# Optimization experiments

Hardware: AMD Instinct MI355X
Metric: run time of the kernel (lower is better)

The kernel has to match this reference:

```python
import jax, jax.numpy as jnp
import numpy as np

EMBED_DIM = 1024
N_HEAD = 16
D_K = EMBED_DIM // N_HEAD


def setup_inputs() -> dict:
    key = jax.random.key(0)
    kq, kk, kv, kwq, kwk, kwv, kwo = jax.random.split(key, 7)
    B, S, E = 4, 2048, EMBED_DIM
    scale = 1.0 / np.sqrt(E)
    return {
        "Q": jax.random.normal(kq, (B, S, E), dtype=jnp.float32),
        "K": jax.random.normal(kk, (B, S, E), dtype=jnp.float32),
        "V": jax.random.normal(kv, (B, S, E), dtype=jnp.float32),
        "mask": jnp.zeros((1,), dtype=jnp.bool_),  # unused by the module's forward
        "Wq": jax.random.normal(kwq, (E, E), dtype=jnp.float32) * scale,
        "Wk": jax.random.normal(kwk, (E, E), dtype=jnp.float32) * scale,
        "Wv": jax.random.normal(kwv, (E, E), dtype=jnp.float32) * scale,
        "Wo": jax.random.normal(kwo, (E, E), dtype=jnp.float32) * scale,
    }


def reference(Q, K, V, mask, Wq, Wk, Wv, Wo):
    B, S, E = Q.shape
    H, Dk = N_HEAD, D_K
    # Linear projections (torch Linear: x @ W.T), split into heads -> [B,H,S,Dk]
    q = (Q @ Wq.T).reshape(B, S, H, Dk).transpose(0, 2, 1, 3)
    k = (K @ Wk.T).reshape(B, S, H, Dk).transpose(0, 2, 1, 3)
    v = (V @ Wv.T).reshape(B, S, H, Dk).transpose(0, 2, 1, 3)
    # Scaled dot-product attention (no mask is passed in the original forward;
    # dropout is identity in eval mode)
    scores = jnp.einsum("bhqd,bhkd->bhqk", q, k) / jnp.sqrt(jnp.float32(Dk))
    attn = jax.nn.softmax(scores, axis=-1)
    ctx = jnp.einsum("bhqk,bhkd->bhqd", attn, v)  # [B,H,S,Dk]
    ctx = ctx.transpose(0, 2, 1, 3).reshape(B, S, E)
    return ctx @ Wo.T
```

## Files before the change

kernel.cpp:

```cpp
#include <hip/hip_runtime.h>
#include <hip/hip_bf16.h>

#define B_  4
#define S_  2048
#define E_  1024
#define H_  16
#define DK_ 64
#define CSC 0.18033688011112042f

using bf16   = __bf16;
using bf16x8 = __attribute__((ext_vector_type(8))) __bf16;
using f32x4  = __attribute__((ext_vector_type(4))) float;

__device__ __forceinline__ f32x4 mfma16(bf16x8 a, bf16x8 b, f32x4 c) {
    return __builtin_amdgcn_mfma_f32_16x16x32_bf16(a, b, c, 0, 0, 0);
}

__device__ __forceinline__ bf16x8 cvt8(float4 a, float4 b) {
    bf16x8 r;
    r[0] = (bf16)a.x; r[1] = (bf16)a.y; r[2] = (bf16)a.z; r[3] = (bf16)a.w;
    r[4] = (bf16)b.x; r[5] = (bf16)b.y; r[6] = (bf16)b.z; r[7] = (bf16)b.w;
    return r;
}

__device__ __forceinline__ void gl16(const void* g, void* l) {
    __builtin_amdgcn_global_load_lds(
        (const __attribute__((address_space(1))) void*)g,
        (__attribute__((address_space(3))) void*)l, 16, 0, 0);
}

__global__ __launch_bounds__(256) void cvtw3(const float* __restrict__ a,
                                             const float* __restrict__ b,
                                             const float* __restrict__ c,
                                             bf16* __restrict__ d, float s0) {
    const int y = blockIdx.y;
    const float* s = y == 0 ? a : y == 1 ? b : c;
    const float sc = y == 0 ? s0 : 1.f;
    const size_t i = (size_t)blockIdx.x * 256 + threadIdx.x;
    float4 u = ((const float4*)s)[i * 2];
    float4 v = ((const float4*)s)[i * 2 + 1];
    u.x *= sc; u.y *= sc; u.z *= sc; u.w *= sc;
    v.x *= sc; v.y *= sc; v.z *= sc; v.w *= sc;
    ((bf16x8*)(d + (size_t)y * E_ * E_))[i] = cvt8(u, v);
}

__global__ __launch_bounds__(256, 3) void gemm_qkv(
    const float* __restrict__ Qi, const float* __restrict__ Ki,
    const float* __restrict__ Vi, const bf16* __restrict__ Wb,
    bf16* __restrict__ qws, bf16* __restrict__ kws, bf16* __restrict__ vtws) {
    __shared__ __align__(16) bf16 sA[128 * 32];
    __shared__ __align__(16) bf16 sB[128 * 32];

    const int t = threadIdx.x;
    const int lane = t & 63, wave = t >> 6;
    const int wm = wave >> 1, wn = wave & 1;
    const int quad = lane >> 4, l16 = lane & 15;

    const int sel = blockIdx.y >> 3;
    const int gm = blockIdx.x * 128;
    const int gn = (blockIdx.y & 7) * 128;

    const float* A = sel == 0 ? Qi : sel == 1 ? Ki : Vi;
    const bf16* W = Wb + (size_t)sel * E_ * E_;

    const int srow = t >> 1, scol = (t & 1) * 16;
    const float* ga = A + (size_t)(gm + srow) * E_ + scol;
    const int cb = (t & 1) * 2, swA = (srow >> 1) & 3;
    bf16* la0 = (bf16*)((char*)sA + srow * 64 + ((cb ^ swA) * 16));
    bf16* la1 = (bf16*)((char*)sA + srow * 64 + (((cb + 1) ^ swA) * 16));

    const int brow = lane >> 2;
    const int bcg  = (lane & 3) ^ ((lane >> 3) & 3);
    const bf16* gB[2];
#pragma unroll
    for (int j = 0; j < 2; ++j)
        gB[j] = W + (size_t)(gn + wave * 32 + j * 16 + brow) * E_ + bcg * 8;

    float4 ra[4];
#pragma unroll
    for (int j = 0; j < 4; ++j) ra[j] = *(const float4*)(ga + j * 4);

    f32x4 acc[4][4];
#pragma unroll
    for (int i = 0; i < 4; ++i)
#pragma unroll
        for (int j = 0; j < 4; ++j) acc[i][j] = f32x4{0.f, 0.f, 0.f, 0.f};

    for (int kt = 0; kt < E_ / 32; ++kt) {
        __syncthreads();
        *(bf16x8*)la0 = cvt8(ra[0], ra[1]);
        *(bf16x8*)la1 = cvt8(ra[2], ra[3]);
#pragma unroll
        for (int j = 0; j < 2; ++j)
            gl16(gB[j] + kt * 32, (char*)sB + (wave * 2 + j) * 1024);
        __syncthreads();
        if (kt + 1 < E_ / 32) {
            const int kk = (kt + 1) * 32;
#pragma unroll
            for (int j = 0; j < 4; ++j)
                ra[j] = *(const float4*)(ga + kk + j * 4);
        }

        bf16x8 Af[4], Bf[4];
#pragma unroll
        for (int ms = 0; ms < 4; ++ms) {
            const int r = wm * 64 + ms * 16 + l16;
            Af[ms] = *(const bf16x8*)((const char*)sA + r * 64 +
                                      ((quad ^ ((r >> 1) & 3)) * 16));
        }
#pragma unroll
        for (int ns = 0; ns < 4; ++ns) {
            const int r = wn * 64 + ns * 16 + l16;
            Bf[ns] = *(const bf16x8*)((const char*)sB + r * 64 +
                                      ((quad ^ ((r >> 1) & 3)) * 16));
        }
#pragma unroll
        for (int ms = 0; ms < 4; ++ms)
#pragma unroll
            for (int ns = 0; ns < 4; ++ns)
                acc[ms][ns] = mfma16(Af[ms], Bf[ns], acc[ms][ns]);
    }

#pragma unroll
    for (int ms = 0; ms < 4; ++ms)
#pragma unroll
        for (int ns = 0; ns < 4; ++ns) {
            const int col = gn + wn * 64 + ns * 16 + l16;
            const int row0 = gm + wm * 64 + ms * 16 + quad * 4;
            const int h = col >> 6, d = col & (DK_ - 1);
#pragma unroll
            for (int r = 0; r < 4; ++r) {
                const int i = row0 + r;
                const int bb = i >> 11, s = i & (S_ - 1);
                const float v = acc[ms][ns][r];
                if (sel == 2)
                    vtws[(((size_t)(bb * H_ + h)) * DK_ + d) * S_ + s] = (bf16)v;
                else if (sel == 1)
                    kws[(((size_t)(bb * H_ + h)) * S_ + s) * DK_ + d] = (bf16)v;
                else
                    qws[(((size_t)(bb * H_ + h)) * S_ + s) * DK_ + d] = (bf16)v;
            }
        }
}

__global__ __launch_bounds__(256, 3) void gemm_out(const bf16* __restrict__ A,
                                                   const bf16* __restrict__ W,
                                                   float* __restrict__ out) {
    __shared__ __align__(16) bf16 sA[128 * 32];
    __shared__ __align__(16) bf16 sB[128 * 32];

    const int t = threadIdx.x;
    const int lane = t & 63, wave = t >> 6;
    const int wm = wave >> 1, wn = wave & 1;
    const int quad = lane >> 4, l16 = lane & 15;
    const int gm = blockIdx.x * 128;
    const int gn = blockIdx.y * 128;

    const int brow = lane >> 2;
    const int bcg  = (lane & 3) ^ ((lane >> 3) & 3);
    const bf16* gA[2];
    const bf16* gB[2];
#pragma unroll
    for (int j = 0; j < 2; ++j) {
        gA[j] = A + (size_t)(gm + wave * 32 + j * 16 + brow) * E_ + bcg * 8;
        gB[j] = W + (size_t)(gn + wave * 32 + j * 16 + brow) * E_ + bcg * 8;
    }

    f32x4 acc[4][4];
#pragma unroll
    for (int i = 0; i < 4; ++i)
#pragma unroll
        for (int j = 0; j < 4; ++j) acc[i][j] = f32x4{0.f, 0.f, 0.f, 0.f};

    for (int kt = 0; kt < E_ / 32; ++kt) {
        __syncthreads();
#pragma unroll
        for (int j = 0; j < 2; ++j) {
            gl16(gA[j] + kt * 32, (char*)sA + (wave * 2 + j) * 1024);
            gl16(gB[j] + kt * 32, (char*)sB + (wave * 2 + j) * 1024);
        }
        __syncthreads();

        bf16x8 Af[4], Bf[4];
#pragma unroll
        for (int ms = 0; ms < 4; ++ms) {
            const int r = wm * 64 + ms * 16 + l16;
            Af[ms] = *(const bf16x8*)((const char*)sA + r * 64 +
                                      ((quad ^ ((r >> 1) & 3)) * 16));
        }
#pragma unroll
        for (int ns = 0; ns < 4; ++ns) {
            const int r = wn * 64 + ns * 16 + l16;
            Bf[ns] = *(const bf16x8*)((const char*)sB + r * 64 +
                                      ((quad ^ ((r >> 1) & 3)) * 16));
        }
#pragma unroll
        for (int ms = 0; ms < 4; ++ms)
#pragma unroll
            for (int ns = 0; ns < 4; ++ns)
                acc[ms][ns] = mfma16(Af[ms], Bf[ns], acc[ms][ns]);
    }

#pragma unroll
    for (int ms = 0; ms < 4; ++ms)
#pragma unroll
        for (int ns = 0; ns < 4; ++ns) {
            const int col = gn + wn * 64 + ns * 16 + l16;
            const int row0 = gm + wm * 64 + ms * 16 + quad * 4;
#pragma unroll
            for (int r = 0; r < 4; ++r)
                out[(size_t)(row0 + r) * E_ + col] = acc[ms][ns][r];
        }
}

#define PSTR 72
__global__ __launch_bounds__(256) void attn4(const bf16* __restrict__ q,
                                             const bf16* __restrict__ k,
                                             const bf16* __restrict__ vt,
                                             bf16* __restrict__ ctx) {
    __shared__ __align__(16) bf16 sK[64 * 64];
    __shared__ __align__(16) bf16 sV[64 * 64];
    __shared__ __align__(16) bf16 plds[4][32 * PSTR];

    const int t = threadIdx.x;
    const int lane = t & 63, wave = t >> 6;
    const int quad = lane >> 4, l16 = lane & 15;
    const int qb = (blockIdx.x * 4 + wave) * 32;
    const int bh = blockIdx.y;
    const size_t base  = (size_t)bh * S_ * DK_;
    const size_t baseT = (size_t)bh * DK_ * S_;
    bf16* pw = &plds[wave][0];

    const int srow = t >> 2, sc4 = (t & 3) * 16;
    const int cb = (t & 3) * 2, swr = srow & 7;
    const bf16* gK = k + base + (size_t)srow * DK_ + sc4;
    const bf16* gV = vt + baseT + (size_t)srow * S_ + sc4;
    char* wK0 = (char*)sK + srow * 128 + ((cb ^ swr) * 16);
    char* wK1 = (char*)sK + srow * 128 + (((cb + 1) ^ swr) * 16);
    char* wV0 = (char*)sV + srow * 128 + ((cb ^ swr) * 16);
    char* wV1 = (char*)sV + srow * 128 + (((cb + 1) ^ swr) * 16);

    bf16x8 rk[2], rv[2];
    rk[0] = *(const bf16x8*)(gK);
    rk[1] = *(const bf16x8*)(gK + 8);
    rv[0] = *(const bf16x8*)(gV);
    rv[1] = *(const bf16x8*)(gV + 8);

    bf16x8 aQ[2][2];
#pragma unroll
    for (int t2 = 0; t2 < 2; ++t2) {
        const bf16* qp = q + base + (size_t)(qb + t2 * 16 + l16) * DK_ + quad * 8;
        aQ[t2][0] = *(const bf16x8*)(qp);
        aQ[t2][1] = *(const bf16x8*)(qp + 32);
    }

    f32x4 acc[2][4];
    float l_i[2][4];
#pragma unroll
    for (int t2 = 0; t2 < 2; ++t2)
#pragma unroll
        for (int nb = 0; nb < 4; ++nb) {
            acc[t2][nb] = f32x4{0.f, 0.f, 0.f, 0.f};
            l_i[t2][nb] = 0.f;
        }

    for (int kt = 0; kt < S_ / 64; ++kt) {
        __syncthreads();
        *(bf16x8*)wK0 = rk[0];
        *(bf16x8*)wK1 = rk[1];
        *(bf16x8*)wV0 = rv[0];
        *(bf16x8*)wV1 = rv[1];
        __syncthreads();
        if (kt + 1 < S_ / 64) {
            const bf16* nK = gK + (size_t)(kt + 1) * 64 * DK_;
            const bf16* nV = gV + (size_t)(kt + 1) * 64;
            rk[0] = *(const bf16x8*)(nK);
            rk[1] = *(const bf16x8*)(nK + 8);
            rv[0] = *(const bf16x8*)(nV);
            rv[1] = *(const bf16x8*)(nV + 8);
        }

        f32x4 sc[2][4];
#pragma unroll
        for (int kb = 0; kb < 4; ++kb) {
            const int r = kb * 16 + l16, sw = r & 7;
            const bf16x8 b0 =
                *(const bf16x8*)((const char*)sK + r * 128 + ((quad ^ sw) * 16));
            const bf16x8 b1 = *(const bf16x8*)((const char*)sK + r * 128 +
                                               (((quad + 4) ^ sw) * 16));
#pragma unroll
            for (int t2 = 0; t2 < 2; ++t2) {
                f32x4 z = f32x4{0.f, 0.f, 0.f, 0.f};
                z = mfma16(aQ[t2][0], b0, z);
                sc[t2][kb] = mfma16(aQ[t2][1], b1, z);
            }
        }

#pragma unroll
        for (int t2 = 0; t2 < 2; ++t2)
#pragma unroll
            for (int r = 0; r < 4; ++r) {
                const int prow = (t2 * 16 + quad * 4 + r) * PSTR;
#pragma unroll
                for (int kb = 0; kb < 4; ++kb) {
                    const float p = __builtin_amdgcn_exp2f(sc[t2][kb][r]);
                    l_i[t2][r] += p;
                    pw[prow + kb * 16 + l16] = (bf16)p;
                }
            }

        bf16x8 aP[2][2];
#pragma unroll
        for (int t2 = 0; t2 < 2; ++t2) {
            aP[t2][0] = *(const bf16x8*)(pw + (t2 * 16 + l16) * PSTR + quad * 8);
            aP[t2][1] = *(const bf16x8*)(pw + (t2 * 16 + l16) * PSTR + 32 + quad * 8);
        }

#pragma unroll
        for (int nb = 0; nb < 4; ++nb) {
            const int r = nb * 16 + l16, sw = r & 7;
            const bf16x8 b0 =
                *(const bf16x8*)((const char*)sV + r * 128 + ((quad ^ sw) * 16));
            const bf16x8 b1 = *(const bf16x8*)((const char*)sV + r * 128 +
                                               (((quad + 4) ^ sw) * 16));
#pragma unroll
            for (int t2 = 0; t2 < 2; ++t2) {
                acc[t2][nb] = mfma16(aP[t2][0], b0, acc[t2][nb]);
                acc[t2][nb] = mfma16(aP[t2][1], b1, acc[t2][nb]);
            }
        }
    }

#pragma unroll
    for (int t2 = 0; t2 < 2; ++t2)
#pragma unroll
        for (int r = 0; r < 4; ++r) {
            float x = l_i[t2][r];
            x += __shfl_xor(x, 1);
            x += __shfl_xor(x, 2);
            x += __shfl_xor(x, 4);
            x += __shfl_xor(x, 8);
            l_i[t2][r] = 1.f / x;
        }

    const int b = bh >> 4, h = bh & (H_ - 1);
#pragma unroll
    for (int t2 = 0; t2 < 2; ++t2)
#pragma unroll
        for (int nb = 0; nb < 4; ++nb)
#pragma unroll
            for (int r = 0; r < 4; ++r) {
                const int s = qb + t2 * 16 + quad * 4 + r;
                const size_t idx =
                    ((size_t)(b * S_ + s)) * E_ + h * DK_ + nb * 16 + l16;
                ctx[idx] = (bf16)(acc[t2][nb][r] * l_i[t2][r]);
            }
}

extern "C" void kernel_launch(void* const* d_in, const int* in_sizes, int n_in,
                              void* d_out, int out_size, void* d_ws,
                              size_t ws_size, hipStream_t stream) {
    const float* Q  = (const float*)d_in[0];
    const float* K  = (const float*)d_in[1];
    const float* V  = (const float*)d_in[2];
    const float* Wq = (const float*)d_in[4];
    const float* Wk = (const float*)d_in[5];
    const float* Wv = (const float*)d_in[6];
    const float* Wo = (const float*)d_in[7];
    float* out = (float*)d_out;

    const size_t NTOK = (size_t)B_ * S_ * E_;
    bf16* qws  = (bf16*)d_ws;
    bf16* kws  = qws + NTOK;
    bf16* vtws = kws + NTOK;
    bf16* cws  = vtws + NTOK;

    bf16* wqkvb = cws;
    bf16* wob   = qws;

    const int CW_BLK = E_ * E_ / 8 / 256;

    cvtw3<<<dim3(CW_BLK, 3), 256, 0, stream>>>(Wq, Wk, Wv, wqkvb, CSC);

    gemm_qkv<<<dim3(B_ * S_ / 128, 24), 256, 0, stream>>>(
        Q, K, V, wqkvb, qws, kws, vtws);

    attn4<<<dim3(S_ / 128, B_ * H_), 256, 0, stream>>>(qws, kws, vtws, cws);

    cvtw3<<<dim3(CW_BLK, 1), 256, 0, stream>>>(Wo, Wo, Wo, wob, 1.f);

    gemm_out<<<dim3(B_ * S_ / 128, E_ / 128), 256, 0, stream>>>(cws, wob, out);
}
```

Baseline: 385.6 us.

## Replace projection GEMMs with 256x256 double-buffered 8-wave bf16 GEMM

Replaces the 128x128 4-wave projection and output GEMMs with a templated 256x256-tile, 512-thread kernel. It double-buffers 64KB LDS stages loaded via global_load_lds, waits with explicit vmcnt/lgkmcnt, and interleaves quarter-tile MFMA phases with setprio. Activations Q/K/V are pre-converted to bf16 in separate passes, using the output buffer as scratch and reusing it for V after the Q/K GEMM. This cuts in-loop fp32 loads and conversion and raises data reuse per tile, at the cost of extra conversion passes, 128KB dynamic LDS and fragile manual synchronisation.

```diff
diff --git a/kernel.cpp b/kernel.cpp
--- a/kernel.cpp
+++ b/kernel.cpp
@@ -27,6 +27,24 @@
     __builtin_amdgcn_global_load_lds(
         (const __attribute__((address_space(1))) void*)g,
         (__attribute__((address_space(3))) void*)l, 16, 0, 0);
+}
+
+#define SBAR()  __builtin_amdgcn_s_barrier()
+#define WV4()  { asm volatile("s_waitcnt vmcnt(4)" ::: "memory");   \
+                 __builtin_amdgcn_sched_barrier(0); }
+#define WL0()  { asm volatile("s_waitcnt lgkmcnt(0)" ::: "memory"); \
+                 __builtin_amdgcn_sched_barrier(0); }
+
+__global__ __launch_bounds__(256) void cvt_pair(const float* __restrict__ a,
+                                                const float* __restrict__ b,
+                                                bf16* __restrict__ da,
+                                                bf16* __restrict__ db) {
+    const float* s = blockIdx.y ? b : a;
+    bf16* d = blockIdx.y ? db : da;
+    const size_t i = (size_t)blockIdx.x * 256 + threadIdx.x;
+    const float4 u = ((const float4*)s)[i * 2];
+    const float4 v = ((const float4*)s)[i * 2 + 1];
+    ((bf16x8*)d)[i] = cvt8(u, v);
 }
 
 __global__ __launch_bounds__(256) void cvtw3(const float* __restrict__ a,
@@ -44,173 +62,159 @@
     ((bf16x8*)(d + (size_t)y * E_ * E_))[i] = cvt8(u, v);
 }
 
-__global__ __launch_bounds__(256, 3) void gemm_qkv(
-    const float* __restrict__ Qi, const float* __restrict__ Ki,
-    const float* __restrict__ Vi, const bf16* __restrict__ Wb,
-    bf16* __restrict__ qws, bf16* __restrict__ kws, bf16* __restrict__ vtws) {
-    __shared__ __align__(16) bf16 sA[128 * 32];
-    __shared__ __align__(16) bf16 sB[128 * 32];
+template <int MODE>
+__global__ __launch_bounds__(512, 2) void gemm8(
+    const bf16* __restrict__ Aq, const bf16* __restrict__ Ak,
+    const bf16* __restrict__ Av, const bf16* __restrict__ Wb,
+    bf16* __restrict__ qws, bf16* __restrict__ kws, bf16* __restrict__ vtws,
+    float* __restrict__ fout, int selbase) {
+    extern __shared__ __align__(16) char sm[];
 
     const int t = threadIdx.x;
-    const int lane = t & 63, wave = t >> 6;
-    const int wm = wave >> 1, wn = wave & 1;
+    const int lane = t & 63, w = t >> 6;
+    const int wm = w >> 2, wn = w & 3;
     const int quad = lane >> 4, l16 = lane & 15;
 
-    const int sel = blockIdx.y >> 3;
-    const int gm = blockIdx.x * 128;
-    const int gn = (blockIdx.y & 7) * 128;
-
-    const float* A = sel == 0 ? Qi : sel == 1 ? Ki : Vi;
-    const bf16* W = Wb + (size_t)sel * E_ * E_;
-
-    const int srow = t >> 1, scol = (t & 1) * 16;
-    const float* ga = A + (size_t)(gm + srow) * E_ + scol;
-    const int cb = (t & 1) * 2, swA = (srow >> 1) & 3;
-    bf16* la0 = (bf16*)((char*)sA + srow * 64 + ((cb ^ swA) * 16));
-    bf16* la1 = (bf16*)((char*)sA + srow * 64 + (((cb + 1) ^ swA) * 16));
-
-    const int brow = lane >> 2;
-    const int bcg  = (lane & 3) ^ ((lane >> 3) & 3);
-    const bf16* gB[2];
-#pragma unroll
-    for (int j = 0; j < 2; ++j)
-        gB[j] = W + (size_t)(gn + wave * 32 + j * 16 + brow) * E_ + bcg * 8;
-
-    float4 ra[4];
-#pragma unroll
-    for (int j = 0; j < 4; ++j) ra[j] = *(const float4*)(ga + j * 4);
-
-    f32x4 acc[4][4];
-#pragma unroll
-    for (int i = 0; i < 4; ++i)
+    int sel, gn;
+    if (MODE == 0) {
+        sel = selbase + (blockIdx.y >> 2);
+        gn = (blockIdx.y & 3) * 256;
+    } else {
+        sel = 0;
+        gn = blockIdx.y * 256;
+    }
+    const int gm = blockIdx.x * 256;
+
+    const bf16* A = (MODE == 1) ? Aq : (sel == 0 ? Aq : sel == 1 ? Ak : Av);
+    const bf16* W = (MODE == 1) ? Wb : Wb + (size_t)sel * E_ * E_;
+
+    const int lr = lane >> 3;
+    const int scw = (lane & 7) ^ lr;
+    const int s0 = w * 2, s1 = s0 + 1;
+    const int arow0 = (s0 >> 3) * 128 + (s0 & 7) * 8;
+    const int arow1 = (s1 >> 3) * 128 + (s1 & 7) * 8;
+    const int brow0 = (s0 >> 2) * 64 + (s0 & 3) * 8;
+    const int brow1 = (s1 >> 2) * 64 + (s1 & 3) * 8;
+
+    const char* gAa0 = (const char*)(A + (size_t)(gm + arow0 + lr) * E_) + scw * 16;
+    const char* gAa1 = (const char*)(A + (size_t)(gm + arow1 + lr) * E_) + scw * 16;
+    const char* gAb0 = gAa0 + (size_t)64 * E_ * 2;
+    const char* gAb1 = gAa1 + (size_t)64 * E_ * 2;
+    const char* gBa0 = (const char*)(W + (size_t)(gn + brow0 + lr) * E_) + scw * 16;
+    const char* gBa1 = (const char*)(W + (size_t)(gn + brow1 + lr) * E_) + scw * 16;
+    const char* gBb0 = gBa0 + (size_t)32 * E_ * 2;
+    const char* gBb1 = gBa1 + (size_t)32 * E_ * 2;
+
+#define STG_Aa(nb, kb) { gl16(gAa0 + (kb), sm + (nb) + arow0 * 128);              \
+                         gl16(gAa1 + (kb), sm + (nb) + arow1 * 128); }
+#define STG_Ab(nb, kb) { gl16(gAb0 + (kb), sm + (nb) + (arow0 + 64) * 128);       \
+                         gl16(gAb1 + (kb), sm + (nb) + (arow1 + 64) * 128); }
+#define STG_Ba(nb, kb) { gl16(gBa0 + (kb), sm + (nb) + 32768 + brow0 * 128);      \
+                         gl16(gBa1 + (kb), sm + (nb) + 32768 + brow1 * 128); }
+#define STG_Bb(nb, kb) { gl16(gBb0 + (kb), sm + (nb) + 32768 + (brow0+32) * 128); \
+                         gl16(gBb1 + (kb), sm + (nb) + 32768 + (brow1+32) * 128); }
+
+    const int cK0 = ((0 * 4 + quad) ^ (l16 & 7)) * 16;
+    const int cK1 = ((1 * 4 + quad) ^ (l16 & 7)) * 16;
+
+    f32x4 acc[8][4];
+#pragma unroll
+    for (int i = 0; i < 8; ++i)
 #pragma unroll
         for (int j = 0; j < 4; ++j) acc[i][j] = f32x4{0.f, 0.f, 0.f, 0.f};
 
-    for (int kt = 0; kt < E_ / 32; ++kt) {
-        __syncthreads();
-        *(bf16x8*)la0 = cvt8(ra[0], ra[1]);
-        *(bf16x8*)la1 = cvt8(ra[2], ra[3]);
-#pragma unroll
-        for (int j = 0; j < 2; ++j)
-            gl16(gB[j] + kt * 32, (char*)sB + (wave * 2 + j) * 1024);
-        __syncthreads();
-        if (kt + 1 < E_ / 32) {
-            const int kk = (kt + 1) * 32;
-#pragma unroll
-            for (int j = 0; j < 4; ++j)
-                ra[j] = *(const float4*)(ga + kk + j * 4);
-        }
-
-        bf16x8 Af[4], Bf[4];
-#pragma unroll
-        for (int ms = 0; ms < 4; ++ms) {
-            const int r = wm * 64 + ms * 16 + l16;
-            Af[ms] = *(const bf16x8*)((const char*)sA + r * 64 +
-                                      ((quad ^ ((r >> 1) & 3)) * 16));
-        }
-#pragma unroll
-        for (int ns = 0; ns < 4; ++ns) {
-            const int r = wn * 64 + ns * 16 + l16;
-            Bf[ns] = *(const bf16x8*)((const char*)sB + r * 64 +
-                                      ((quad ^ ((r >> 1) & 3)) * 16));
-        }
-#pragma unroll
-        for (int ms = 0; ms < 4; ++ms)
-#pragma unroll
-            for (int ns = 0; ns < 4; ++ns)
-                acc[ms][ns] = mfma16(Af[ms], Bf[ns], acc[ms][ns]);
-    }
-
-#pragma unroll
-    for (int ms = 0; ms < 4; ++ms)
-#pragma unroll
-        for (int ns = 0; ns < 4; ++ns) {
-            const int col = gn + wn * 64 + ns * 16 + l16;
-            const int row0 = gm + wm * 64 + ms * 16 + quad * 4;
-            const int h = col >> 6, d = col & (DK_ - 1);
-#pragma unroll
-            for (int r = 0; r < 4; ++r) {
-                const int i = row0 + r;
-                const int bb = i >> 11, s = i & (S_ - 1);
-                const float v = acc[ms][ns][r];
-                if (sel == 2)
-                    vtws[(((size_t)(bb * H_ + h)) * DK_ + d) * S_ + s] = (bf16)v;
-                else if (sel == 1)
-                    kws[(((size_t)(bb * H_ + h)) * S_ + s) * DK_ + d] = (bf16)v;
-                else
-                    qws[(((size_t)(bb * H_ + h)) * S_ + s) * DK_ + d] = (bf16)v;
+    bf16x8 Af[4][2], Bf[2][2];
+
+#define LDA(cb, MH)                                                            \
+    _Pragma("unroll") for (int ml = 0; ml < 4; ++ml) {                         \
+        const int rb = (wm * 128 + (MH) * 64 + ml * 16 + l16) * 128;           \
+        Af[ml][0] = *(const bf16x8*)(sm + (cb) + rb + cK0);                    \
+        Af[ml][1] = *(const bf16x8*)(sm + (cb) + rb + cK1);                    \
+    }
+#define LDB(cb, NH)                                                            \
+    _Pragma("unroll") for (int nl = 0; nl < 2; ++nl) {                         \
+        const int rb = (wn * 64 + (NH) * 32 + nl * 16 + l16) * 128;            \
+        Bf[nl][0] = *(const bf16x8*)(sm + (cb) + 32768 + rb + cK0);            \
+        Bf[nl][1] = *(const bf16x8*)(sm + (cb) + 32768 + rb + cK1);            \
+    }
+#define MFMAQ(MH, NH)                                                          \
+    __builtin_amdgcn_s_setprio(1);                                             \
+    _Pragma("unroll") for (int ml = 0; ml < 4; ++ml)                           \
+    _Pragma("unroll") for (int nl = 0; nl < 2; ++nl) {                         \
+        acc[(MH)*4+ml][(NH)*2+nl] =                                            \
+            mfma16(Af[ml][0], Bf[nl][0], acc[(MH)*4+ml][(NH)*2+nl]);           \
+        acc[(MH)*4+ml][(NH)*2+nl] =                                            \
+            mfma16(Af[ml][1], Bf[nl][1], acc[(MH)*4+ml][(NH)*2+nl]);           \
+    }                                                                          \
+    __builtin_amdgcn_s_setprio(0);
+
+    STG_Aa(0, 0); STG_Ba(0, 0); STG_Bb(0, 0); STG_Ab(0, 0);
+    WV4();
+    SBAR();
+
+    for (int kt = 0; kt < 16; ++kt) {
+        const size_t cb = (size_t)(kt & 1) * 65536;
+        const size_t nb = cb ^ 65536;
+        const size_t kb = (size_t)(kt + 1 < 16 ? kt + 1 : 15) * 128;
+
+        LDA(cb, 0); LDB(cb, 0);
+        STG_Aa(nb, kb);
+        WV4(); SBAR(); WL0();
+        MFMAQ(0, 0);
+        SBAR();
+
+        LDB(cb, 1);
+        STG_Ba(nb, kb);
+        WV4(); SBAR(); WL0();
+        MFMAQ(0, 1);
+        SBAR();
+
+        LDA(cb, 1);
+        STG_Bb(nb, kb);
+        SBAR(); WL0();
+        MFMAQ(1, 1);
+        SBAR();
+
+        LDB(cb, 0);
+        STG_Ab(nb, kb);
+        WV4(); SBAR(); WL0();
+        MFMAQ(1, 0);
+        SBAR();
+    }
+
+#pragma unroll
+    for (int mf = 0; mf < 8; ++mf)
+#pragma unroll
+        for (int nf = 0; nf < 4; ++nf) {
+            const int col = gn + wn * 64 + nf * 16 + l16;
+            const int row0 = gm + wm * 128 + mf * 16 + quad * 4;
+            if (MODE == 1) {
+#pragma unroll
+                for (int r = 0; r < 4; ++r)
+                    fout[(size_t)(row0 + r) * E_ + col] = acc[mf][nf][r];
+            } else {
+                const int h = col >> 6, d = col & (DK_ - 1);
+#pragma unroll
+                for (int r = 0; r < 4; ++r) {
+                    const int i = row0 + r;
+                    const int bb = i >> 11, s = i & (S_ - 1);
+                    const float v = acc[mf][nf][r];
+                    if (sel == 2)
+                        vtws[(((size_t)(bb * H_ + h)) * DK_ + d) * S_ + s] = (bf16)v;
+                    else if (sel == 1)
+                        kws[(((size_t)(bb * H_ + h)) * S_ + s) * DK_ + d] = (bf16)v;
+                    else
+                        qws[(((size_t)(bb * H_ + h)) * S_ + s) * DK_ + d] = (bf16)v;
+                }
             }
         }
-}
-
-__global__ __launch_bounds__(256, 3) void gemm_out(const bf16* __restrict__ A,
-                                                   const bf16* __restrict__ W,
-                                                   float* __restrict__ out) {
-    __shared__ __align__(16) bf16 sA[128 * 32];
-    __shared__ __align__(16) bf16 sB[128 * 32];
-
-    const int t = threadIdx.x;
-    const int lane = t & 63, wave = t >> 6;
-    const int wm = wave >> 1, wn = wave & 1;
-    const int quad = lane >> 4, l16 = lane & 15;
-    const int gm = blockIdx.x * 128;
-    const int gn = blockIdx.y * 128;
-
-    const int brow = lane >> 2;
-    const int bcg  = (lane & 3) ^ ((lane >> 3) & 3);
-    const bf16* gA[2];
-    const bf16* gB[2];
-#pragma unroll
-    for (int j = 0; j < 2; ++j) {
-        gA[j] = A + (size_t)(gm + wave * 32 + j * 16 + brow) * E_ + bcg * 8;
-        gB[j] = W + (size_t)(gn + wave * 32 + j * 16 + brow) * E_ + bcg * 8;
-    }
-
-    f32x4 acc[4][4];
-#pragma unroll
-    for (int i = 0; i < 4; ++i)
-#pragma unroll
-        for (int j = 0; j < 4; ++j) acc[i][j] = f32x4{0.f, 0.f, 0.f, 0.f};
-
-    for (int kt = 0; kt < E_ / 32; ++kt) {
-        __syncthreads();
-#pragma unroll
-        for (int j = 0; j < 2; ++j) {
-            gl16(gA[j] + kt * 32, (char*)sA + (wave * 2 + j) * 1024);
-            gl16(gB[j] + kt * 32, (char*)sB + (wave * 2 + j) * 1024);
-        }
-        __syncthreads();
-
-        bf16x8 Af[4], Bf[4];
-#pragma unroll
-        for (int ms = 0; ms < 4; ++ms) {
-            const int r = wm * 64 + ms * 16 + l16;
-            Af[ms] = *(const bf16x8*)((const char*)sA + r * 64 +
-                                      ((quad ^ ((r >> 1) & 3)) * 16));
-        }
-#pragma unroll
-        for (int ns = 0; ns < 4; ++ns) {
-            const int r = wn * 64 + ns * 16 + l16;
-            Bf[ns] = *(const bf16x8*)((const char*)sB + r * 64 +
-                                      ((quad ^ ((r >> 1) & 3)) * 16));
-        }
-#pragma unroll
-        for (int ms = 0; ms < 4; ++ms)
-#pragma unroll
-            for (int ns = 0; ns < 4; ++ns)
-                acc[ms][ns] = mfma16(Af[ms], Bf[ns], acc[ms][ns]);
-    }
-
-#pragma unroll
-    for (int ms = 0; ms < 4; ++ms)
-#pragma unroll
-        for (int ns = 0; ns < 4; ++ns) {
-            const int col = gn + wn * 64 + ns * 16 + l16;
-            const int row0 = gm + wm * 64 + ms * 16 + quad * 4;
-#pragma unroll
-            for (int r = 0; r < 4; ++r)
-                out[(size_t)(row0 + r) * E_ + col] = acc[ms][ns][r];
-        }
+#undef STG_Aa
+#undef STG_Ab
+#undef STG_Ba
+#undef STG_Bb
+#undef LDA
+#undef LDB
+#undef MFMAQ
 }
 
 #define PSTR 72
@@ -377,17 +381,25 @@
 
     bf16* wqkvb = cws;
     bf16* wob   = qws;
-
-    const int CW_BLK = E_ * E_ / 8 / 256;
-
-    cvtw3<<<dim3(CW_BLK, 3), 256, 0, stream>>>(Wq, Wk, Wv, wqkvb, CSC);
-
-    gemm_qkv<<<dim3(B_ * S_ / 128, 24), 256, 0, stream>>>(
-        Q, K, V, wqkvb, qws, kws, vtws);
+    bf16* Qb = (bf16*)d_out;
+    bf16* Kb = Qb + NTOK;
+    bf16* Vb = Qb;
+
+    cvt_pair<<<dim3(4096, 2), 256, 0, stream>>>(Q, K, Qb, Kb);
+    cvtw3<<<dim3(512, 3), 256, 0, stream>>>(Wq, Wk, Wv, wqkvb, CSC);
+
+    gemm8<0><<<dim3(32, 8), 512, 131072, stream>>>(
+        Qb, Kb, Vb, wqkvb, qws, kws, vtws, nullptr, 0);
+
+    cvt_pair<<<dim3(4096, 1), 256, 0, stream>>>(V, V, Vb, Vb);
+
+    gemm8<0><<<dim3(32, 4), 512, 131072, stream>>>(
+        Qb, Kb, Vb, wqkvb, qws, kws, vtws, nullptr, 2);
 
     attn4<<<dim3(S_ / 128, B_ * H_), 256, 0, stream>>>(qws, kws, vtws, cws);
 
-    cvtw3<<<dim3(CW_BLK, 1), 256, 0, stream>>>(Wo, Wo, Wo, wob, 1.f);
-
-    gemm_out<<<dim3(B_ * S_ / 128, E_ / 128), 256, 0, stream>>>(cws, wob, out);
-}
+    cvtw3<<<dim3(512, 1), 256, 0, stream>>>(Wo, Wo, Wo, wob, 1.f);
+
+    gemm8<1><<<dim3(32, 4), 512, 131072, stream>>>(
+        cws, cws, cws, wob, nullptr, nullptr, nullptr, out, 0);
+}
```

After: 385.9 us. About the same (+0.1%).
